# Optimization experiments

Hardware: AMD Instinct MI355X
Metric: run time of the kernel (lower is better)

## Reference

```python
import jax, jax.numpy as jnp
import numpy as np
import math

D_MODEL = 1024
NUM_HEADS = 16
D_HEAD = D_MODEL // NUM_HEADS          # 64
N_FREQ = D_HEAD // 2 + 1               # 33 rfft bins
COMPRESSION_RATIO = 0.5


def setup_inputs() -> dict:
    key = jax.random.key(0)
    k_x, k_qkv, k_out, k_b, k_m = jax.random.split(key, 5)
    B, S = 2, 2048
    x = jax.random.normal(k_x, (B, S, D_MODEL), dtype=jnp.float32)
    # Linear weights stored as [in, out] (torch Linear uses [out, in]; math identical).
    w_qkv = jax.random.normal(k_qkv, (D_MODEL, 3 * D_MODEL), dtype=jnp.float32) / math.sqrt(D_MODEL)
    w_out = jax.random.normal(k_out, (D_MODEL, D_MODEL), dtype=jnp.float32) / math.sqrt(D_MODEL)
    b_out = jax.random.normal(k_b, (D_MODEL,), dtype=jnp.float32) * 0.01
    # Learned per-frequency-bin mask logits of AdaptiveFrequencyMask(d_state=d_head).
    # Initialized around logit(compression_ratio) with small noise.
    init_logit = math.log(COMPRESSION_RATIO / (1.0 - COMPRESSION_RATIO))
    mask_logits = init_logit + 0.1 * jax.random.normal(k_m, (N_FREQ,), dtype=jnp.float32)
    return {"x": x, "w_qkv": w_qkv, "w_out": w_out, "b_out": b_out, "mask_logits": mask_logits}


def _spectral_filter(t, mask):
    # rfft over d_head dim, apply learned soft mask, inverse rfft.  t: [B,H,S,dh]
    tf = jnp.fft.rfft(t, axis=-1)          # [B,H,S,N_FREQ] complex
    tf = tf * mask                          # broadcast real mask over bins
    return jnp.fft.irfft(tf, n=t.shape[-1], axis=-1).astype(t.dtype)


def reference(x, w_qkv, w_out, b_out, mask_logits):
    B, S, D = x.shape
    H, dh = NUM_HEADS, D_HEAD
    qkv = x @ w_qkv                                         # [B,S,3D]
    q, k, v = jnp.split(qkv, 3, axis=-1)
    # [B,S,D] -> [B,H,S,dh]
    to_heads = lambda t: t.reshape(B, S, H, dh).transpose(0, 2, 1, 3)
    q, k, v = to_heads(q), to_heads(k), to_heads(v)
    mask = jax.nn.sigmoid(mask_logits)                      # [N_FREQ]
    q = _spectral_filter(q, mask)
    k = _spectral_filter(k, mask)
    scores = jnp.einsum('bhqd,bhkd->bhqk', q, k) / math.sqrt(dh)
    attn = jax.nn.softmax(scores, axis=-1)                  # dropout p=0 (eval)
    out = jnp.einsum('bhqk,bhkd->bhqd', attn, v)
    out = out.transpose(0, 2, 1, 3).reshape(B, S, D)
    return out @ w_out + b_out
```

## Files before the change

### kernel.cpp

```cpp
#include <hip/hip_runtime.h>

#define S_LEN 2048
#define NH    16
#define DH    64
#define DM    1024
#define NQKV  3072

typedef __attribute__((ext_vector_type(8))) __bf16 bf16x8;
typedef __attribute__((ext_vector_type(4))) float  f32x4;
typedef unsigned short ushort_t;

static __device__ __forceinline__ unsigned short bf16b(float f) {
  return __builtin_bit_cast(unsigned short, (__bf16)f);
}

static __device__ __forceinline__ float exp2v(float x) {
  return __builtin_amdgcn_exp2f(x);
}

static __device__ __forceinline__ bf16x8 pack8(float4 f0, float4 f1) {
  uint4 v;
  v.x = ((unsigned)bf16b(f0.y) << 16) | bf16b(f0.x);
  v.y = ((unsigned)bf16b(f0.w) << 16) | bf16b(f0.z);
  v.z = ((unsigned)bf16b(f1.y) << 16) | bf16b(f1.x);
  v.w = ((unsigned)bf16b(f1.w) << 16) | bf16b(f1.z);
  return __builtin_bit_cast(bf16x8, v);
}

static __device__ __forceinline__ void glds16(const void* g, void* l) {
  __builtin_amdgcn_global_load_lds((const __attribute__((address_space(1))) unsigned int*)g,
                                   (__attribute__((address_space(3))) unsigned int*)l, 16, 0, 0);
}

#define OFF_WT  65536ull
#define OFF_WOT 6356992ull
#define OFF_Q   8454144ull
#define OFF_K   16842752ull
#define OFF_V   25231360ull
#define OFF_AO  33619968ull

__global__ __launch_bounds__(256) void k_prep(const float* __restrict__ wqkv,
                                              const float* __restrict__ wout,
                                              const float* __restrict__ x,
                                              const float* __restrict__ logits,
                                              unsigned short* __restrict__ Wt,
                                              unsigned short* __restrict__ Wot,
                                              unsigned short* __restrict__ xb) {
  __shared__ __align__(16) char sbuf[16640];
  int bid = blockIdx.x;
  int t = threadIdx.x;

  if (bid < 256) {
    float* msk = (float*)sbuf;
    float* Kd  = (float*)(sbuf + 144);
    ushort_t (*Fb)[72] = (ushort_t(*)[72])(sbuf + 416);
    if (t < 33) msk[t] = 1.0f / (1.0f + __expf(-logits[t]));
    __syncthreads();
    if (t < 64) {
      float acc = msk[0];
      #pragma unroll
      for (int f = 1; f < 32; ++f) {
        int r = (f * t) & 63;
        acc += 2.0f * msk[f] * __cosf((float)r * (6.28318530717958647692f / 64.0f));
      }
      acc += msk[32] * ((t & 1) ? -1.0f : 1.0f);
      Kd[t] = acc * (1.0f / 64.0f);
    }
    __syncthreads();
    for (int idx = t; idx < 4096; idx += 256) {
      int j = idx >> 6, i = idx & 63;
      Fb[j][i] = bf16b(Kd[(j - i) & 63]);
    }
    __syncthreads();

    int lane = t & 63, w = t >> 6;
    int m16 = lane & 15, quad = lane >> 4;
    int kx = bid >> 5, yy = bid & 31;
    int which = yy >> 4, h = yy & 15;
    int base = which * 1024 + h * 64;

    bf16x8 af0 = *(const bf16x8*)(&Fb[w * 16 + m16][quad * 8]);
    bf16x8 af1 = *(const bf16x8*)(&Fb[w * 16 + m16][32 + quad * 8]);

    f32x4 acc[8] = {};
    #pragma unroll 2
    for (int n = 0; n < 8; ++n) {
      const float* Wg = wqkv + (size_t)(kx * 128 + n * 16 + m16) * NQKV + base + quad * 8;
      float4 a0 = *(const float4*)(Wg);
      float4 a1 = *(const float4*)(Wg + 4);
      float4 b0 = *(const float4*)(Wg + 32);
      float4 b1 = *(const float4*)(Wg + 36);
      acc[n] = __builtin_amdgcn_mfma_f32_16x16x32_bf16(af0, pack8(a0, a1), acc[n], 0, 0, 0);
      acc[n] = __builtin_amdgcn_mfma_f32_16x16x32_bf16(af1, pack8(b0, b1), acc[n], 0, 0, 0);
    }
    float sc = (which == 0) ? 0.18033688011112042f : 1.0f;
    #pragma unroll
    for (int n = 0; n < 8; ++n) {
      #pragma unroll
      for (int r = 0; r < 4; ++r) {
        int j = w * 16 + quad * 4 + r;
        Wt[(size_t)(base + j) * DM + kx * 128 + n * 16 + m16] = bf16b(acc[n][r] * sc);
      }
    }
  } else if (bid < 768) {
    float (*Ts)[65] = (float(*)[65])sbuf;
    int b1 = bid - 256;
    if (b1 < 256) {
      int kt = b1 & 15, nt = b1 >> 4;
      int cb = 2048 + nt * 64, kbase = kt * 64;
      #pragma unroll
      for (int p = 0; p < 16; ++p) {
        int kk = p * 4 + (t >> 6);
        Ts[kk][t & 63] = wqkv[(size_t)(kbase + kk) * NQKV + cb + (t & 63)];
      }
      __syncthreads();
      #pragma unroll
      for (int p = 0; p < 16; ++p) {
        int nn = p * 4 + (t >> 6);
        Wt[(size_t)(cb + nn) * DM + kbase + (t & 63)] = bf16b(Ts[t & 63][nn]);
      }
    } else {
      int b2 = b1 - 256;
      int kt = b2 & 15, nt = b2 >> 4;
      int cb = nt * 64, kbase = kt * 64;
      #pragma unroll
      for (int p = 0; p < 16; ++p) {
        int kk = p * 4 + (t >> 6);
        Ts[kk][t & 63] = wout[(size_t)(kbase + kk) * DM + cb + (t & 63)];
      }
      __syncthreads();
      #pragma unroll
      for (int p = 0; p < 16; ++p) {
        int nn = p * 4 + (t >> 6);
        Wot[(size_t)(cb + nn) * DM + kbase + (t & 63)] = bf16b(Ts[t & 63][nn]);
      }
    }
  } else {
    size_t i = ((size_t)(bid - 768) * 256 + t) * 8;
    const float4* xp = (const float4*)(x + i);
    float4 a = xp[0], b = xp[1];
    uint4 v;
    v.x = ((unsigned)bf16b(a.y) << 16) | bf16b(a.x);
    v.y = ((unsigned)bf16b(a.w) << 16) | bf16b(a.z);
    v.z = ((unsigned)bf16b(b.y) << 16) | bf16b(b.x);
    v.w = ((unsigned)bf16b(b.w) << 16) | bf16b(b.z);
    *(uint4*)(xb + i) = v;
  }
}

template<int BM, int BN, int WCOLS, int MR, int NR>
__device__ __forceinline__ void gemm_core2(const unsigned short* __restrict__ A,
                                           const unsigned short* __restrict__ Bw,
                                           int bm, int bn, unsigned short* smem,
                                           f32x4 (&acc)[MR][NR]) {
  constexpr int SLOT = (BM + BN) * 64;
  constexpr int PA = BM / 64, PB = BN / 64;
  constexpr int L = PA + PB;
  int t = threadIdx.x, lane = t & 63, w = t >> 6;
  int m16 = lane & 15, quad = lane >> 4;
  int wr = (w / WCOLS) * (MR * 16), wc = (w % WCOLS) * (NR * 16);
  int xr = m16 & 7;
  int trow = t >> 3, tcol = t & 7;
  int gsw = (tcol ^ (trow & 7)) * 8;
  const unsigned short* Ag = A  + (size_t)(bm * BM + trow) * DM + gsw;
  const unsigned short* Bg = Bw + (size_t)(bn * BN + trow) * DM + gsw;
  unsigned short* Al = smem + trow * 64 + tcol * 8;
  unsigned short* Bl = smem + BM * 64 + trow * 64 + tcol * 8;

  #pragma unroll
  for (int s = 0; s < 2; ++s) {
    #pragma unroll
    for (int p = 0; p < PA; ++p)
      glds16(Ag + (size_t)p * 64 * DM + s * 64, Al + s * SLOT + p * 4096);
    #pragma unroll
    for (int p = 0; p < PB; ++p)
      glds16(Bg + (size_t)p * 64 * DM + s * 64, Bl + s * SLOT + p * 4096);
  }

  #pragma unroll 1
  for (int ks = 0; ks < 16; ++ks) {
    if (ks < 15) asm volatile("s_waitcnt vmcnt(%0)" :: "n"(L) : "memory");
    else         asm volatile("s_waitcnt vmcnt(0)" ::: "memory");
    __builtin_amdgcn_s_barrier();
    __builtin_amdgcn_sched_barrier(0);
    const unsigned short* As = smem + (ks & 1) * SLOT;
    const unsigned short* Bs = As + BM * 64;
    #pragma unroll
    for (int kk = 0; kk < 2; ++kk) {
      bf16x8 af[MR], bfr[NR];
      #pragma unroll
      for (int i = 0; i < MR; ++i)
        af[i] = *(const bf16x8*)(As + (wr + i * 16 + m16) * 64 + ((kk * 4 + quad) ^ xr) * 8);
      #pragma unroll
      for (int j = 0; j < NR; ++j)
        bfr[j] = *(const bf16x8*)(Bs + (wc + j * 16 + m16) * 64 + ((kk * 4 + quad) ^ xr) * 8);
      #pragma unroll
      for (int i = 0; i < MR; ++i)
        #pragma unroll
        for (int j = 0; j < NR; ++j)
          acc[i][j] = __builtin_amdgcn_mfma_f32_16x16x32_bf16(af[i], bfr[j], acc[i][j], 0, 0, 0);
    }
    if (ks < 14) {
      __builtin_amdgcn_s_barrier();
      __builtin_amdgcn_sched_barrier(0);
      int kn = ks + 2;
      #pragma unroll
      for (int p = 0; p < PA; ++p)
        glds16(Ag + (size_t)p * 64 * DM + kn * 64, Al + (ks & 1) * SLOT + p * 4096);
      #pragma unroll
      for (int p = 0; p < PB; ++p)
        glds16(Bg + (size_t)p * 64 * DM + kn * 64, Bl + (ks & 1) * SLOT + p * 4096);
    }
  }
  __syncthreads();
}

__global__ __launch_bounds__(512, 1) void k_gemm_qkv(const unsigned short* __restrict__ xb,
                                                     const unsigned short* __restrict__ Bw,
                                                     unsigned short* __restrict__ Qb,
                                                     unsigned short* __restrict__ Kb,
                                                     unsigned short* __restrict__ Vt) {
  __shared__ __align__(16) unsigned short smem[57344];
  f32x4 acc[8][3] = {};
  int bn = blockIdx.x, bm = blockIdx.y;
  gemm_core2<256, 192, 4, 8, 3>(xb, Bw, bm, bn, smem, acc);

  int t = threadIdx.x, lane = t & 63, w = t >> 6;
  int m16 = lane & 15, quad = lane >> 4;
  int wr = (w >> 2) * 128, wc = (w & 3) * 48;
  int b = bm >> 3, srow = (bm & 7) * 256;
  ushort_t (*Tr)[200] = (ushort_t(*)[200])smem;

  #pragma unroll
  for (int i = 0; i < 8; ++i)
    #pragma unroll
    for (int j = 0; j < 3; ++j)
      #pragma unroll
      for (int r = 0; r < 4; ++r)
        Tr[wr + i * 16 + quad * 4 + r][wc + j * 16 + m16] = bf16b(acc[i][j][r]);
  __syncthreads();

  #pragma unroll
  for (int ch = 0; ch < 3; ++ch) {
    int cb = bn * 192 + ch * 64;
    int which = cb >> 10, hcol = (cb >> 6) & 15;
    if (which < 2) {
      int row = t >> 1, part = t & 1;
      unsigned short* dst = (which ? Kb : Qb) +
          ((size_t)(b * 16 + hcol) * 2048 + srow + row) * 64 + part * 32;
      #pragma unroll
      for (int p = 0; p < 4; ++p)
        *(uint4*)(dst + p * 8) = *(const uint4*)(&Tr[row][ch * 64 + part * 32 + p * 8]);
    } else {
      int d = t & 63, rb = (t >> 6) * 32;
      unsigned short* dst = Vt + ((size_t)(b * 16 + hcol) * 64 + d) * 2048 + srow + rb;
      #pragma unroll
      for (int p = 0; p < 4; ++p) {
        unsigned short tmp[8];
        #pragma unroll
        for (int q = 0; q < 8; ++q) tmp[q] = Tr[rb + p * 8 + q][ch * 64 + d];
        *(uint4*)(dst + p * 8) = *(const uint4*)tmp;
      }
    }
  }
}

__global__ __launch_bounds__(512, 2) void k_attn(const unsigned short* __restrict__ Qb,
                                                 const unsigned short* __restrict__ Kb,
                                                 const unsigned short* __restrict__ Vt,
                                                 unsigned short* __restrict__ AO) {
  __shared__ __align__(16) unsigned short smem[65536];
  int t = threadIdx.x;
  int w = t >> 6, lane = t & 63;
  int m16 = lane & 15, quad = lane >> 4;
  int bid = blockIdx.x;
  int jj = bid >> 3;
  int bh = ((jj & 3) << 3) + (bid & 7);
  int qbase = (jj >> 2) * 256 + w * 32;

  const unsigned short* QpA = Qb + ((size_t)bh * S_LEN + qbase + m16) * DH + quad * 8;
  const unsigned short* QpB = QpA + 16 * DH;
  bf16x8 aq0A = *(const bf16x8*)(QpA);
  bf16x8 aq1A = *(const bf16x8*)(QpA + 32);
  bf16x8 aq0B = *(const bf16x8*)(QpB);
  bf16x8 aq1B = *(const bf16x8*)(QpB + 32);
  const unsigned short* Kbase = Kb + (size_t)bh * S_LEN * DH;
  const unsigned short* Vbase = Vt + (size_t)bh * DH * S_LEN;

  int xr = m16 & 7;
  int krow0 = ((m16 >> 2) << 3) + (m16 & 3);

  int trow = t >> 3;
  int tcol = t & 7;
  int gswzK = tcol ^ ((trow & 3) | ((trow >> 1) & 4));
  int gswzV = tcol ^ (trow & 7);
  const unsigned short* Kg = Kbase + (size_t)trow * 64 + gswzK * 8;
  const unsigned short* Vg = Vbase + (size_t)trow * S_LEN + gswzV * 8;
  unsigned short* Kl = smem + trow * 64 + tcol * 8;
  unsigned short* Vl = smem + 32768 + trow * 64 + tcol * 8;

  f32x4 oA[4] = {}, oB[4] = {};
  float lA = 0.f, lB = 0.f;
  f32x4 zero = {0.f, 0.f, 0.f, 0.f};

  #pragma unroll
  for (int tt = 0; tt < 6; ++tt) {
    glds16(Kg + (size_t)tt * 4096, Kl + tt * 4096);
    glds16(Vg + tt * 64,           Vl + tt * 4096);
  }

#define QK_TILE(KSH, SA, SB)                                                              \
    _Pragma("unroll")                                                                     \
    for (int c = 0; c < 2; ++c) {                                                         \
      _Pragma("unroll")                                                                   \
      for (int gl = 0; gl < 2; ++gl) {                                                    \
        int key = c * 32 + krow0 + gl * 4;                                                \
        bf16x8 kf0 = *(const bf16x8*)((KSH) + key * 64 + ((quad ^ xr) * 8));              \
        bf16x8 kf1 = *(const bf16x8*)((KSH) + key * 64 + (((4 + quad) ^ xr) * 8));        \
        SA[c][gl] = __builtin_amdgcn_mfma_f32_16x16x32_bf16(kf0, aq0A, zero, 0, 0, 0);    \
        SA[c][gl] = __builtin_amdgcn_mfma_f32_16x16x32_bf16(kf1, aq1A, SA[c][gl], 0, 0, 0);\
        SB[c][gl] = __builtin_amdgcn_mfma_f32_16x16x32_bf16(kf0, aq0B, zero, 0, 0, 0);    \
        SB[c][gl] = __builtin_amdgcn_mfma_f32_16x16x32_bf16(kf1, aq1B, SB[c][gl], 0, 0, 0);\
      }                                                                                   \
    }

#define SM_TILE(SA, SB, PA_, PB_)                                                         \
    _Pragma("unroll")                                                                     \
    for (int c = 0; c < 2; ++c) {                                                         \
      float a0 = exp2v(SA[c][0][0]), a1 = exp2v(SA[c][0][1]);                             \
      float a2 = exp2v(SA[c][0][2]), a3 = exp2v(SA[c][0][3]);                             \
      float a4 = exp2v(SA[c][1][0]), a5 = exp2v(SA[c][1][1]);                             \
      float a6 = exp2v(SA[c][1][2]), a7 = exp2v(SA[c][1][3]);                             \
      lA += ((a0 + a1) + (a2 + a3)) + ((a4 + a5) + (a6 + a7));                            \
      uint4 ua;                                                                           \
      ua.x = ((unsigned)bf16b(a1) << 16) | bf16b(a0);                                     \
      ua.y = ((unsigned)bf16b(a3) << 16) | bf16b(a2);                                     \
      ua.z = ((unsigned)bf16b(a5) << 16) | bf16b(a4);                                     \
      ua.w = ((unsigned)bf16b(a7) << 16) | bf16b(a6);                                     \
      PA_[c] = __builtin_bit_cast(bf16x8, ua);                                            \
      float b0 = exp2v(SB[c][0][0]), b1 = exp2v(SB[c][0][1]);                             \
      float b2 = exp2v(SB[c][0][2]), b3 = exp2v(SB[c][0][3]);                             \
      float b4 = exp2v(SB[c][1][0]), b5 = exp2v(SB[c][1][1]);                             \
      float b6 = exp2v(SB[c][1][2]), b7 = exp2v(SB[c][1][3]);                             \
      lB += ((b0 + b1) + (b2 + b3)) + ((b4 + b5) + (b6 + b7));                            \
      uint4 ub;                                                                           \
      ub.x = ((unsigned)bf16b(b1) << 16) | bf16b(b0);                                     \
      ub.y = ((unsigned)bf16b(b3) << 16) | bf16b(b2);                                     \
      ub.z = ((unsigned)bf16b(b5) << 16) | bf16b(b4);                                     \
      ub.w = ((unsigned)bf16b(b7) << 16) | bf16b(b6);                                     \
      PB_[c] = __builtin_bit_cast(bf16x8, ub);                                            \
    }

#define PV_TILE(VSH, PA_, PB_)                                                            \
    _Pragma("unroll")                                                                     \
    for (int c = 0; c < 2; ++c) {                                                         \
      _Pragma("unroll")                                                                   \
      for (int j = 0; j < 4; ++j) {                                                       \
        int dv = j * 16 + m16;                                                            \
        bf16x8 bv = *(const bf16x8*)((VSH) + dv * 64 + (((c * 4 + quad) ^ xr) * 8));      \
        oA[j] = __builtin_amdgcn_mfma_f32_16x16x32_bf16(PA_[c], bv, oA[j], 0, 0, 0);      \
        oB[j] = __builtin_amdgcn_mfma_f32_16x16x32_bf16(PB_[c], bv, oB[j], 0, 0, 0);      \
      }                                                                                   \
    }

  #pragma unroll 1
  for (int wnd = 0; wnd < 16; ++wnd) {
    if (wnd < 14)      asm volatile("s_waitcnt vmcnt(8)" ::: "memory");
    else if (wnd < 15) asm volatile("s_waitcnt vmcnt(4)" ::: "memory");
    else               asm volatile("s_waitcnt vmcnt(0)" ::: "memory");
    __builtin_amdgcn_s_barrier();
    __builtin_amdgcn_sched_barrier(0);
    if (wnd < 13) {
      int ta = 2 * wnd + 6;
      glds16(Kg + (size_t)ta * 4096,       Kl + (ta & 7) * 4096);
      glds16(Vg + ta * 64,                 Vl + (ta & 7) * 4096);
      glds16(Kg + (size_t)(ta + 1) * 4096, Kl + ((ta + 1) & 7) * 4096);
      glds16(Vg + (ta + 1) * 64,           Vl + ((ta + 1) & 7) * 4096);
    }
    int s0 = (2 * wnd) & 7, s1 = (2 * wnd + 1) & 7;
    const unsigned short* Ka  = smem + s0 * 4096;
    const unsigned short* Kbs = smem + s1 * 4096;
    const unsigned short* Va  = smem + 32768 + s0 * 4096;
    const unsigned short* Vbs = smem + 32768 + s1 * 4096;

    f32x4 sA[2][2], sB[2][2];
    __builtin_amdgcn_s_setprio(1);
    QK_TILE(Ka, sA, sB)
    __builtin_amdgcn_s_setprio(0);
    bf16x8 paA[2], paB[2];
    SM_TILE(sA, sB, paA, paB)
    f32x4 tA[2][2], tB[2][2];
    __builtin_amdgcn_s_setprio(1);
    QK_TILE(Kbs, tA, tB)
    PV_TILE(Va, paA, paB)
    __builtin_amdgcn_s_setprio(0);
    bf16x8 pbA[2], pbB[2];
    SM_TILE(tA, tB, pbA, pbB)
    __builtin_amdgcn_s_setprio(1);
    PV_TILE(Vbs, pbA, pbB)
    __builtin_amdgcn_s_setprio(0);
  }
#undef QK_TILE
#undef SM_TILE
#undef PV_TILE

  lA += __shfl_xor(lA, 16); lA += __shfl_xor(lA, 32);
  lB += __shfl_xor(lB, 16); lB += __shfl_xor(lB, 32);
  float ivA = 1.0f / lA;
  float ivB = 1.0f / lB;
  int b = bh >> 4, h = bh & 15;
  #pragma unroll
  for (int r = 0; r < 4; ++r) {
    float vA = __shfl(ivA, quad * 4 + r);
    float vB = __shfl(ivB, quad * 4 + r);
    size_t row0 = (size_t)b * S_LEN + qbase + quad * 4 + r;
    unsigned short* d0 = AO + row0 * DM + h * DH + m16;
    unsigned short* d1 = AO + (row0 + 16) * DM + h * DH + m16;
    #pragma unroll
    for (int j = 0; j < 4; ++j) {
      d0[j * 16] = bf16b(oA[j][r] * vA);
      d1[j * 16] = bf16b(oB[j][r] * vB);
    }
  }
}

__global__ __launch_bounds__(512, 1) void k_gemm_out(const unsigned short* __restrict__ A,
                                                     const unsigned short* __restrict__ Bw,
                                                     const float* __restrict__ bias,
                                                     float* __restrict__ out) {
  __shared__ __align__(16) unsigned short smem[32768];
  f32x4 acc[4][2] = {};
  int bn = blockIdx.x, bm = blockIdx.y;
  gemm_core2<128, 128, 4, 4, 2>(A, Bw, bm, bn, smem, acc);

  int t = threadIdx.x, lane = t & 63, w = t >> 6;
  int m16 = lane & 15, quad = lane >> 4;
  int wr = (w >> 2) * 64, wc = (w & 3) * 32;
  #pragma unroll
  for (int i = 0; i < 4; ++i) {
    int grow = bm * 128 + wr + i * 16 + quad * 4;
    #pragma unroll
    for (int j = 0; j < 2; ++j) {
      int gc = bn * 128 + wc + j * 16 + m16;
      float bb = bias[gc];
      #pragma unroll
      for (int r = 0; r < 4; ++r)
        out[(size_t)(grow + r) * DM + gc] = acc[i][j][r] + bb;
    }
  }
}

extern "C" void kernel_launch(void* const* d_in, const int* in_sizes, int n_in,
                              void* d_out, int out_size, void* d_ws, size_t ws_size,
                              hipStream_t stream) {
  const float* x    = (const float*)d_in[0];
  const float* wqkv = (const float*)d_in[1];
  const float* wout = (const float*)d_in[2];
  const float* bout = (const float*)d_in[3];
  const float* mlog = (const float*)d_in[4];
  char* ws = (char*)d_ws;
  unsigned short* Wt  = (unsigned short*)(ws + OFF_WT);
  unsigned short* Wot = (unsigned short*)(ws + OFF_WOT);
  unsigned short* Qb  = (unsigned short*)(ws + OFF_Q);
  unsigned short* Kb  = (unsigned short*)(ws + OFF_K);
  unsigned short* Vt  = (unsigned short*)(ws + OFF_V);
  unsigned short* xb  = (unsigned short*)(ws + OFF_AO);
  unsigned short* AO  = (unsigned short*)(ws + OFF_AO);
  float* out = (float*)d_out;

  k_prep<<<dim3(2816), dim3(256), 0, stream>>>(wqkv, wout, x, mlog, Wt, Wot, xb);
  k_gemm_qkv<<<dim3(16, 16), dim3(512), 0, stream>>>(xb, Wt, Qb, Kb, Vt);
  k_attn<<<dim3(256), dim3(512), 0, stream>>>(Qb, Kb, Vt, AO);
  k_gemm_out<<<dim3(8, 32), dim3(512), 0, stream>>>(AO, Wot, bout, out);
}
```

Before: 185.6 us.

## Give each attention wave 64 query rows with 4 warps and smaller LDS ring

The attention kernel drops from 8 to 4 waves per block, and each wave now handles 64 query rows (four 16-row fragments) instead of 32. Every K/V fragment read from LDS is therefore reused across four MFMA query tiles, which halves LDS reads per FLOP. The K/V ring buffer shrinks from 8 slots to 4, and the loop processes one 64-key tile per iteration instead of two interleaved tiles. In exchange, register pressure rises (16 output accumulators plus scores), and the software pipelining that overlapped QK of one tile with PV of the previous tile is lost.

```diff
diff --git a/kernel.cpp b/kernel.cpp
--- a/kernel.cpp
+++ b/kernel.cpp
@@ -265,161 +265,142 @@
   }
 }
 
-__global__ __launch_bounds__(512, 2) void k_attn(const unsigned short* __restrict__ Qb,
+__global__ __launch_bounds__(256, 2) void k_attn(const unsigned short* __restrict__ Qb,
                                                  const unsigned short* __restrict__ Kb,
                                                  const unsigned short* __restrict__ Vt,
                                                  unsigned short* __restrict__ AO) {
-  __shared__ __align__(16) unsigned short smem[65536];
+  __shared__ __align__(16) unsigned short smem[32768];
   int t = threadIdx.x;
   int w = t >> 6, lane = t & 63;
   int m16 = lane & 15, quad = lane >> 4;
   int bid = blockIdx.x;
   int jj = bid >> 3;
   int bh = ((jj & 3) << 3) + (bid & 7);
-  int qbase = (jj >> 2) * 256 + w * 32;
-
-  const unsigned short* QpA = Qb + ((size_t)bh * S_LEN + qbase + m16) * DH + quad * 8;
-  const unsigned short* QpB = QpA + 16 * DH;
-  bf16x8 aq0A = *(const bf16x8*)(QpA);
-  bf16x8 aq1A = *(const bf16x8*)(QpA + 32);
-  bf16x8 aq0B = *(const bf16x8*)(QpB);
-  bf16x8 aq1B = *(const bf16x8*)(QpB + 32);
+  int qbase = (jj >> 2) * 256 + w * 64;
+
+  const unsigned short* Qp = Qb + ((size_t)bh * S_LEN + qbase + m16) * DH + quad * 8;
+  bf16x8 aq0[4], aq1[4];
+  #pragma unroll
+  for (int f = 0; f < 4; ++f) {
+    aq0[f] = *(const bf16x8*)(Qp + f * 16 * DH);
+    aq1[f] = *(const bf16x8*)(Qp + f * 16 * DH + 32);
+  }
   const unsigned short* Kbase = Kb + (size_t)bh * S_LEN * DH;
   const unsigned short* Vbase = Vt + (size_t)bh * DH * S_LEN;
 
   int xr = m16 & 7;
   int krow0 = ((m16 >> 2) << 3) + (m16 & 3);
 
-  int trow = t >> 3;
-  int tcol = t & 7;
-  int gswzK = tcol ^ ((trow & 3) | ((trow >> 1) & 4));
-  int gswzV = tcol ^ (trow & 7);
-  const unsigned short* Kg = Kbase + (size_t)trow * 64 + gswzK * 8;
-  const unsigned short* Vg = Vbase + (size_t)trow * S_LEN + gswzV * 8;
-  unsigned short* Kl = smem + trow * 64 + tcol * 8;
-  unsigned short* Vl = smem + 32768 + trow * 64 + tcol * 8;
-
-  f32x4 oA[4] = {}, oB[4] = {};
-  float lA = 0.f, lB = 0.f;
+  const unsigned short* KgA[2];
+  const unsigned short* VgA[2];
+  unsigned short* KlA[2];
+  unsigned short* VlA[2];
+  #pragma unroll
+  for (int i = 0; i < 2; ++i) {
+    int tt = t + i * 256;
+    int trow = tt >> 3, tcol = tt & 7;
+    int fK = (trow & 3) | ((trow >> 1) & 4);
+    KgA[i] = Kbase + (size_t)trow * 64 + (tcol ^ fK) * 8;
+    VgA[i] = Vbase + (size_t)trow * S_LEN + (tcol ^ (trow & 7)) * 8;
+    KlA[i] = smem + tt * 8;
+    VlA[i] = smem + 16384 + tt * 8;
+  }
+
+  f32x4 o[4][4] = {};
+  float l[4] = {0.f, 0.f, 0.f, 0.f};
   f32x4 zero = {0.f, 0.f, 0.f, 0.f};
 
   #pragma unroll
-  for (int tt = 0; tt < 6; ++tt) {
-    glds16(Kg + (size_t)tt * 4096, Kl + tt * 4096);
-    glds16(Vg + tt * 64,           Vl + tt * 4096);
-  }
-
-#define QK_TILE(KSH, SA, SB)                                                              \
-    _Pragma("unroll")                                                                     \
-    for (int c = 0; c < 2; ++c) {                                                         \
-      _Pragma("unroll")                                                                   \
-      for (int gl = 0; gl < 2; ++gl) {                                                    \
-        int key = c * 32 + krow0 + gl * 4;                                                \
-        bf16x8 kf0 = *(const bf16x8*)((KSH) + key * 64 + ((quad ^ xr) * 8));              \
-        bf16x8 kf1 = *(const bf16x8*)((KSH) + key * 64 + (((4 + quad) ^ xr) * 8));        \
-        SA[c][gl] = __builtin_amdgcn_mfma_f32_16x16x32_bf16(kf0, aq0A, zero, 0, 0, 0);    \
-        SA[c][gl] = __builtin_amdgcn_mfma_f32_16x16x32_bf16(kf1, aq1A, SA[c][gl], 0, 0, 0);\
-        SB[c][gl] = __builtin_amdgcn_mfma_f32_16x16x32_bf16(kf0, aq0B, zero, 0, 0, 0);    \
-        SB[c][gl] = __builtin_amdgcn_mfma_f32_16x16x32_bf16(kf1, aq1B, SB[c][gl], 0, 0, 0);\
-      }                                                                                   \
-    }
-
-#define SM_TILE(SA, SB, PA_, PB_)                                                         \
-    _Pragma("unroll")                                                                     \
-    for (int c = 0; c < 2; ++c) {                                                         \
-      float a0 = exp2v(SA[c][0][0]), a1 = exp2v(SA[c][0][1]);                             \
-      float a2 = exp2v(SA[c][0][2]), a3 = exp2v(SA[c][0][3]);                             \
-      float a4 = exp2v(SA[c][1][0]), a5 = exp2v(SA[c][1][1]);                             \
-      float a6 = exp2v(SA[c][1][2]), a7 = exp2v(SA[c][1][3]);                             \
-      lA += ((a0 + a1) + (a2 + a3)) + ((a4 + a5) + (a6 + a7));                            \
-      uint4 ua;                                                                           \
-      ua.x = ((unsigned)bf16b(a1) << 16) | bf16b(a0);                                     \
-      ua.y = ((unsigned)bf16b(a3) << 16) | bf16b(a2);                                     \
-      ua.z = ((unsigned)bf16b(a5) << 16) | bf16b(a4);                                     \
-      ua.w = ((unsigned)bf16b(a7) << 16) | bf16b(a6);                                     \
-      PA_[c] = __builtin_bit_cast(bf16x8, ua);                                            \
-      float b0 = exp2v(SB[c][0][0]), b1 = exp2v(SB[c][0][1]);                             \
-      float b2 = exp2v(SB[c][0][2]), b3 = exp2v(SB[c][0][3]);                             \
-      float b4 = exp2v(SB[c][1][0]), b5 = exp2v(SB[c][1][1]);                             \
-      float b6 = exp2v(SB[c][1][2]), b7 = exp2v(SB[c][1][3]);                             \
-      lB += ((b0 + b1) + (b2 + b3)) + ((b4 + b5) + (b6 + b7));                            \
-      uint4 ub;                                                                           \
-      ub.x = ((unsigned)bf16b(b1) << 16) | bf16b(b0);                                     \
-      ub.y = ((unsigned)bf16b(b3) << 16) | bf16b(b2);                                     \
-      ub.z = ((unsigned)bf16b(b5) << 16) | bf16b(b4);                                     \
-      ub.w = ((unsigned)bf16b(b7) << 16) | bf16b(b6);                                     \
-      PB_[c] = __builtin_bit_cast(bf16x8, ub);                                            \
-    }
-
-#define PV_TILE(VSH, PA_, PB_)                                                            \
-    _Pragma("unroll")                                                                     \
-    for (int c = 0; c < 2; ++c) {                                                         \
-      _Pragma("unroll")                                                                   \
-      for (int j = 0; j < 4; ++j) {                                                       \
-        int dv = j * 16 + m16;                                                            \
-        bf16x8 bv = *(const bf16x8*)((VSH) + dv * 64 + (((c * 4 + quad) ^ xr) * 8));      \
-        oA[j] = __builtin_amdgcn_mfma_f32_16x16x32_bf16(PA_[c], bv, oA[j], 0, 0, 0);      \
-        oB[j] = __builtin_amdgcn_mfma_f32_16x16x32_bf16(PB_[c], bv, oB[j], 0, 0, 0);      \
-      }                                                                                   \
-    }
+  for (int tt = 0; tt < 3; ++tt) {
+    #pragma unroll
+    for (int i = 0; i < 2; ++i) {
+      glds16(KgA[i] + (size_t)tt * 4096, KlA[i] + tt * 4096);
+      glds16(VgA[i] + tt * 64,           VlA[i] + tt * 4096);
+    }
+  }
 
   #pragma unroll 1
-  for (int wnd = 0; wnd < 16; ++wnd) {
-    if (wnd < 14)      asm volatile("s_waitcnt vmcnt(8)" ::: "memory");
-    else if (wnd < 15) asm volatile("s_waitcnt vmcnt(4)" ::: "memory");
-    else               asm volatile("s_waitcnt vmcnt(0)" ::: "memory");
+  for (int kt = 0; kt < 32; ++kt) {
+    if (kt < 30)      asm volatile("s_waitcnt vmcnt(8)" ::: "memory");
+    else if (kt < 31) asm volatile("s_waitcnt vmcnt(4)" ::: "memory");
+    else              asm volatile("s_waitcnt vmcnt(0)" ::: "memory");
     __builtin_amdgcn_s_barrier();
     __builtin_amdgcn_sched_barrier(0);
-    if (wnd < 13) {
-      int ta = 2 * wnd + 6;
-      glds16(Kg + (size_t)ta * 4096,       Kl + (ta & 7) * 4096);
-      glds16(Vg + ta * 64,                 Vl + (ta & 7) * 4096);
-      glds16(Kg + (size_t)(ta + 1) * 4096, Kl + ((ta + 1) & 7) * 4096);
-      glds16(Vg + (ta + 1) * 64,           Vl + ((ta + 1) & 7) * 4096);
-    }
-    int s0 = (2 * wnd) & 7, s1 = (2 * wnd + 1) & 7;
-    const unsigned short* Ka  = smem + s0 * 4096;
-    const unsigned short* Kbs = smem + s1 * 4096;
-    const unsigned short* Va  = smem + 32768 + s0 * 4096;
-    const unsigned short* Vbs = smem + 32768 + s1 * 4096;
-
-    f32x4 sA[2][2], sB[2][2];
+    if (kt < 29) {
+      int ta = kt + 3, sl = ta & 3;
+      #pragma unroll
+      for (int i = 0; i < 2; ++i) {
+        glds16(KgA[i] + (size_t)ta * 4096, KlA[i] + sl * 4096);
+        glds16(VgA[i] + ta * 64,           VlA[i] + sl * 4096);
+      }
+    }
+    const unsigned short* Ksh = smem + (kt & 3) * 4096;
+    const unsigned short* Vsh = smem + 16384 + (kt & 3) * 4096;
+
+    bf16x8 p[4][2];
+    #pragma unroll
+    for (int c = 0; c < 2; ++c) {
+      f32x4 s[4][2];
+      __builtin_amdgcn_s_setprio(1);
+      #pragma unroll
+      for (int gl = 0; gl < 2; ++gl) {
+        int key = c * 32 + krow0 + gl * 4;
+        bf16x8 kf0 = *(const bf16x8*)(Ksh + key * 64 + ((quad ^ xr) * 8));
+        bf16x8 kf1 = *(const bf16x8*)(Ksh + key * 64 + (((4 + quad) ^ xr) * 8));
+        #pragma unroll
+        for (int f = 0; f < 4; ++f) {
+          s[f][gl] = __builtin_amdgcn_mfma_f32_16x16x32_bf16(kf0, aq0[f], zero, 0, 0, 0);
+          s[f][gl] = __builtin_amdgcn_mfma_f32_16x16x32_bf16(kf1, aq1[f], s[f][gl], 0, 0, 0);
+        }
+      }
+      __builtin_amdgcn_s_setprio(0);
+      #pragma unroll
+      for (int f = 0; f < 4; ++f) {
+        float e0 = exp2v(s[f][0][0]), e1 = exp2v(s[f][0][1]);
+        float e2 = exp2v(s[f][0][2]), e3 = exp2v(s[f][0][3]);
+        float e4 = exp2v(s[f][1][0]), e5 = exp2v(s[f][1][1]);
+        float e6 = exp2v(s[f][1][2]), e7 = exp2v(s[f][1][3]);
+        l[f] += ((e0 + e1) + (e2 + e3)) + ((e4 + e5) + (e6 + e7));
+        uint4 u;
+        u.x = ((unsigned)bf16b(e1) << 16) | bf16b(e0);
+        u.y = ((unsigned)bf16b(e3) << 16) | bf16b(e2);
+        u.z = ((unsigned)bf16b(e5) << 16) | bf16b(e4);
+        u.w = ((unsigned)bf16b(e7) << 16) | bf16b(e6);
+        p[f][c] = __builtin_bit_cast(bf16x8, u);
+      }
+    }
     __builtin_amdgcn_s_setprio(1);
-    QK_TILE(Ka, sA, sB)
+    #pragma unroll
+    for (int c = 0; c < 2; ++c) {
+      #pragma unroll
+      for (int j = 0; j < 4; ++j) {
+        int dv = j * 16 + m16;
+        bf16x8 bv = *(const bf16x8*)(Vsh + dv * 64 + (((c * 4 + quad) ^ xr) * 8));
+        #pragma unroll
+        for (int f = 0; f < 4; ++f)
+          o[f][j] = __builtin_amdgcn_mfma_f32_16x16x32_bf16(p[f][c], bv, o[f][j], 0, 0, 0);
+      }
+    }
     __builtin_amdgcn_s_setprio(0);
-    bf16x8 paA[2], paB[2];
-    SM_TILE(sA, sB, paA, paB)
-    f32x4 tA[2][2], tB[2][2];
-    __builtin_amdgcn_s_setprio(1);
-    QK_TILE(Kbs, tA, tB)
-    PV_TILE(Va, paA, paB)
-    __builtin_amdgcn_s_setprio(0);
-    bf16x8 pbA[2], pbB[2];
-    SM_TILE(tA, tB, pbA, pbB)
-    __builtin_amdgcn_s_setprio(1);
-    PV_TILE(Vbs, pbA, pbB)
-    __builtin_amdgcn_s_setprio(0);
-  }
-#undef QK_TILE
-#undef SM_TILE
-#undef PV_TILE
-
-  lA += __shfl_xor(lA, 16); lA += __shfl_xor(lA, 32);
-  lB += __shfl_xor(lB, 16); lB += __shfl_xor(lB, 32);
-  float ivA = 1.0f / lA;
-  float ivB = 1.0f / lB;
+  }
+
+  #pragma unroll
+  for (int f = 0; f < 4; ++f) {
+    l[f] += __shfl_xor(l[f], 16);
+    l[f] += __shfl_xor(l[f], 32);
+  }
   int b = bh >> 4, h = bh & 15;
   #pragma unroll
-  for (int r = 0; r < 4; ++r) {
-    float vA = __shfl(ivA, quad * 4 + r);
-    float vB = __shfl(ivB, quad * 4 + r);
-    size_t row0 = (size_t)b * S_LEN + qbase + quad * 4 + r;
-    unsigned short* d0 = AO + row0 * DM + h * DH + m16;
-    unsigned short* d1 = AO + (row0 + 16) * DM + h * DH + m16;
-    #pragma unroll
-    for (int j = 0; j < 4; ++j) {
-      d0[j * 16] = bf16b(oA[j][r] * vA);
-      d1[j * 16] = bf16b(oB[j][r] * vB);
+  for (int f = 0; f < 4; ++f) {
+    float iv = 1.0f / l[f];
+    #pragma unroll
+    for (int r = 0; r < 4; ++r) {
+      float v0 = __shfl(iv, quad * 4 + r);
+      size_t row0 = (size_t)b * S_LEN + qbase + f * 16 + quad * 4 + r;
+      unsigned short* d0 = AO + row0 * DM + h * DH + m16;
+      #pragma unroll
+      for (int j = 0; j < 4; ++j)
+        d0[j * 16] = bf16b(o[f][j][r] * v0);
     }
   }
 }
@@ -470,6 +451,6 @@
 
   k_prep<<<dim3(2816), dim3(256), 0, stream>>>(wqkv, wout, x, mlog, Wt, Wot, xb);
   k_gemm_qkv<<<dim3(16, 16), dim3(512), 0, stream>>>(xb, Wt, Qb, Kb, Vt);
-  k_attn<<<dim3(256), dim3(512), 0, stream>>>(Qb, Kb, Vt, AO);
+  k_attn<<<dim3(256), dim3(256), 0, stream>>>(Qb, Kb, Vt, AO);
   k_gemm_out<<<dim3(8, 32), dim3(512), 0, stream>>>(AO, Wot, bout, out);
 }
```

Result: slower. 191.7 us (+3.3%).
